# Kernel optimization log

Hardware: AMD Instinct MI355X
Metric: run time of the kernel (lower is better)

## Reference

```python
import jax, jax.numpy as jnp
import numpy as np

SCALE_VALUE = 1  # init kwarg; divide scores by sqrt(scale_value)


def setup_inputs() -> dict:
    key = jax.random.key(0)
    k1, k2 = jax.random.split(key)
    B, S, D = 8, 4096, 128
    inputs = jax.random.normal(k1, (B, S, D), dtype=jnp.float32)
    kernel = jax.random.normal(k2, (3, D, D), dtype=jnp.float32) * 0.05
    return {"inputs": inputs, "kernel": kernel}


def reference(inputs, kernel):
    # Q/K/V projections: [B,S,D] @ [D,D]
    wq = jnp.einsum('bsd,de->bse', inputs, kernel[0])
    wk = jnp.einsum('bsd,de->bse', inputs, kernel[1])
    wv = jnp.einsum('bsd,de->bse', inputs, kernel[2])
    # full attention score matrix [B,S,S], scaled by 1/sqrt(scale_value)
    qk = jnp.einsum('bqd,bkd->bqk', wq, wk) / (SCALE_VALUE ** 0.5)
    attn = jax.nn.softmax(qk, axis=-1)
    v = jnp.einsum('bqk,bkd->bqd', attn, wv)
    # mean pool over sequence -> [B,D]
    return jnp.mean(v, axis=1)
```

## Files before the change

kernel.cpp:

```cpp
#include <hip/hip_runtime.h>

#define Bsz 8
#define Ssz 4096
#define Dsz 128

typedef short bf16x8 __attribute__((ext_vector_type(8)));
typedef float f32x4 __attribute__((ext_vector_type(4)));
typedef float f32x16 __attribute__((ext_vector_type(16)));
typedef int i32x2 __attribute__((ext_vector_type(2)));
typedef int i32x4 __attribute__((ext_vector_type(4)));
typedef unsigned int u32;

union B8 { u32 u[4]; bf16x8 v; };

__device__ __forceinline__ u32 pkbf(float a, float b) {
  u32 ra = __float_as_uint(a) + 0x8000u;
  u32 rb = __float_as_uint(b) + 0x8000u;
  return __builtin_amdgcn_perm(rb, ra, 0x07060302u);
}
__device__ __forceinline__ short f2bf(float f) {
  u32 r = __float_as_uint(f) + 0x8000u;
  return (short)(r >> 16);
}

__device__ __forceinline__ void gll16(const void* g, void* l) {
  __builtin_amdgcn_global_load_lds((const __attribute__((address_space(1))) void*)g,
                                   (__attribute__((address_space(3))) void*)l, 16, 0, 0);
}


__global__ __launch_bounds__(256, 2) void proj_kernel(
    const float* __restrict__ x, const float* __restrict__ wsrc,
    short* __restrict__ Qs, short* __restrict__ Ks, short* __restrict__ Vp) {
  __shared__ short ob[8192];

  const int rb = blockIdx.x;
  const int t = threadIdx.x;
  const int wv = t >> 6, lane = t & 63, l31 = lane & 31, h = lane >> 5;

  bf16x8 xf[2][8];
  {
    const float* xs = x + (size_t)rb * 64 * Dsz;
    #pragma unroll
    for (int st = 0; st < 2; ++st)
      #pragma unroll
      for (int c = 0; c < 8; ++c) {
        const float* p = xs + (st * 32 + l31) * Dsz + c * 16 + 8 * h;
        f32x4 v0 = *(const f32x4*)p;
        f32x4 v1 = *(const f32x4*)(p + 4);
        B8 tmp;
        tmp.u[0] = pkbf(v0[0], v0[1]); tmp.u[1] = pkbf(v0[2], v0[3]);
        tmp.u[2] = pkbf(v1[0], v1[1]); tmp.u[3] = pkbf(v1[2], v1[3]);
        xf[st][c] = tmp.v;
      }
  }

  for (int mat = 0; mat < 3; ++mat) {
    const float* wm = wsrc + (size_t)mat * Dsz * Dsz;
    const float scale = (mat == 0) ? 1.44269504088896340736f : 1.0f;
    bf16x8 wf[8];
    #pragma unroll
    for (int c = 0; c < 8; ++c) {
      const float* p = wm + (size_t)(c * 16 + 8 * h) * Dsz + wv * 32 + l31;
      B8 tmp;
      #pragma unroll
      for (int j = 0; j < 4; ++j)
        tmp.u[j] = pkbf(p[(2 * j) * Dsz] * scale, p[(2 * j + 1) * Dsz] * scale);
      wf[c] = tmp.v;
    }

    if (mat < 2) {
      #pragma unroll
      for (int st = 0; st < 2; ++st) {
        f32x16 acc = {};
        #pragma unroll
        for (int c = 0; c < 8; ++c)
          acc = __builtin_amdgcn_mfma_f32_32x32x16_bf16(wf[c], xf[st][c], acc, 0, 0, 0);
        #pragma unroll
        for (int g = 0; g < 4; ++g) {
          int e0 = wv * 32 + 8 * g + 4 * h;
          int s = st * 32 + l31;
          i32x2 pr;
          pr[0] = pkbf(acc[4 * g + 0], acc[4 * g + 1]);
          pr[1] = pkbf(acc[4 * g + 2], acc[4 * g + 3]);
          *(i32x2*)&ob[(e0 >> 3) * 512 + s * 8 + (e0 & 7)] = pr;
        }
      }
    } else {
      #pragma unroll
      for (int st = 0; st < 2; ++st) {
        f32x16 acc = {};
        #pragma unroll
        for (int c = 0; c < 8; ++c)
          acc = __builtin_amdgcn_mfma_f32_32x32x16_bf16(xf[st][c], wf[c], acc, 0, 0, 0);
        int e = wv * 32 + l31;
        #pragma unroll
        for (int r = 0; r < 16; ++r) {
          int s = st * 32 + (r & 3) + 8 * (r >> 2) + 4 * h;
          ob[s * 128 + e] = f2bf(acc[r]);
        }
      }
    }
    __syncthreads();
    short* dst = (mat == 0 ? Qs : mat == 1 ? Ks : Vp) + (size_t)rb * 8192;
    #pragma unroll
    for (int p = 0; p < 4; ++p)
      *(i32x4*)&dst[(p * 256 + t) * 8] = *(const i32x4*)&ob[(p * 256 + t) * 8];
    __syncthreads();
  }
}

__global__ __launch_bounds__(256, 2) void lsum_kernel(
    const short* __restrict__ Qs, const short* __restrict__ Ks,
    float* __restrict__ lpart) {
  __shared__ short kbuf[2][8192];

  const int b = blockIdx.x, qt = blockIdx.y, kt = blockIdx.z;
  const int t = threadIdx.x;
  const int wv = t >> 6, lane = t & 63, l31 = lane & 31, h = lane >> 5;

  bf16x8 qf[2][8];
  {
    const short* qsrc = Qs + (size_t)(b * 64 + qt * 4 + wv) * 8192;
    #pragma unroll
    for (int nq = 0; nq < 2; ++nq)
      #pragma unroll
      for (int c = 0; c < 8; ++c)
        qf[nq][c] = *(const bf16x8*)&qsrc[(2 * c + h) * 512 + (nq * 32 + l31) * 8];
  }
  float rs2[2] = {0.f, 0.f};

  const char* kbase = (const char*)(Ks + (size_t)(b * 64 + kt * 16) * 8192);
  #define STAGE_K(it_, bf_)                                                     \
    { const char* src_ = kbase + (size_t)(it_) * 16384;                         \
      _Pragma("unroll")                                                         \
      for (int i_ = 0; i_ < 4; ++i_) {                                          \
        int p_ = wv * 4 + i_;                                                   \
        gll16(src_ + p_ * 1024 + lane * 16, (char*)kbuf[bf_] + p_ * 1024);      \
      } }

  STAGE_K(0, 0);
  __syncthreads();

  for (int it = 0; it < 16; ++it) {
    const int cur = it & 1;
    if (it < 15) STAGE_K(it + 1, cur ^ 1);
    #pragma unroll
    for (int mk = 0; mk < 2; ++mk) {
      bf16x8 kf[8];
      #pragma unroll
      for (int c = 0; c < 8; ++c)
        kf[c] = *(const bf16x8*)&kbuf[cur][(2 * c + h) * 512 + (mk * 32 + l31) * 8];
      f32x16 s0 = {}, s1 = {};
      #pragma unroll
      for (int c = 0; c < 8; ++c) {
        s0 = __builtin_amdgcn_mfma_f32_32x32x16_bf16(kf[c], qf[0][c], s0, 0, 0, 0);
        s1 = __builtin_amdgcn_mfma_f32_32x32x16_bf16(kf[c], qf[1][c], s1, 0, 0, 0);
      }
      #pragma unroll
      for (int r = 0; r < 16; ++r) rs2[0] += __builtin_amdgcn_exp2f(s0[r]);
      #pragma unroll
      for (int r = 0; r < 16; ++r) rs2[1] += __builtin_amdgcn_exp2f(s1[r]);
    }
    __syncthreads();
  }

  #pragma unroll
  for (int nq = 0; nq < 2; ++nq) {
    float v = rs2[nq] + __shfl_xor(rs2[nq], 32, 64);
    if (h == 0)
      lpart[((size_t)kt * 8 + b) * 4096 + qt * 256 + wv * 64 + nq * 32 + l31] = v;
  }
}

__global__ __launch_bounds__(256, 2) void attnv_kernel(
    const short* __restrict__ Qs, const short* __restrict__ Ks,
    const short* __restrict__ Vp, const float* __restrict__ lpart,
    float* __restrict__ partials) {
  __shared__ short kbuf[2][8192];
  __shared__ float linv_lds[256];
  __shared__ float gw[4][1024];
  __shared__ float pwb[512];

  const int b = blockIdx.x, qt = blockIdx.y, kt = blockIdx.z;
  const int t = threadIdx.x;
  const int wv = t >> 6, lane = t & 63, l31 = lane & 31, h = lane >> 5;

  {
    int q = qt * 256 + t;
    float l = lpart[(size_t)b * 4096 + q] + lpart[((size_t)1 * 8 + b) * 4096 + q] +
              lpart[((size_t)2 * 8 + b) * 4096 + q] + lpart[((size_t)3 * 8 + b) * 4096 + q];
    linv_lds[t] = 1.f / (l * (float)Ssz);
  }

  bf16x8 qf[2][8];
  {
    const short* qsrc = Qs + (size_t)(b * 64 + qt * 4 + wv) * 8192;
    #pragma unroll
    for (int mq = 0; mq < 2; ++mq)
      #pragma unroll
      for (int c = 0; c < 8; ++c)
        qf[mq][c] = *(const bf16x8*)&qsrc[(2 * c + h) * 512 + (mq * 32 + l31) * 8];
  }
  __syncthreads();

  float li[2][16];
  #pragma unroll
  for (int mq = 0; mq < 2; ++mq)
    #pragma unroll
    for (int r = 0; r < 16; ++r)
      li[mq][r] = linv_lds[wv * 64 + mq * 32 + (r & 3) + 8 * (r >> 2) + 4 * h];

  const char* kbase = (const char*)(Ks + (size_t)(b * 64 + kt * 16) * 8192);
  STAGE_K(0, 0);
  __syncthreads();

  for (int it = 0; it < 16; ++it) {
    const int cur = it & 1;
    if (it < 15) STAGE_K(it + 1, cur ^ 1);
    #pragma unroll
    for (int nk = 0; nk < 2; ++nk) {
      bf16x8 kf[8];
      #pragma unroll
      for (int c = 0; c < 8; ++c)
        kf[c] = *(const bf16x8*)&kbuf[cur][(2 * c + h) * 512 + (nk * 32 + l31) * 8];
      f32x16 s0 = {}, s1 = {};
      #pragma unroll
      for (int c = 0; c < 8; ++c) {
        s0 = __builtin_amdgcn_mfma_f32_32x32x16_bf16(qf[0][c], kf[c], s0, 0, 0, 0);
        s1 = __builtin_amdgcn_mfma_f32_32x32x16_bf16(qf[1][c], kf[c], s1, 0, 0, 0);
      }
      float gp = 0.f;
      #pragma unroll
      for (int r = 0; r < 16; ++r)
        gp += li[0][r] * __builtin_amdgcn_exp2f(s0[r]) +
              li[1][r] * __builtin_amdgcn_exp2f(s1[r]);
      gp += __shfl_xor(gp, 32, 64);
      if (h == 0) gw[wv][it * 64 + nk * 32 + l31] = gp;
    }
    __syncthreads();
  }

  #pragma unroll
  for (int j = 0; j < 4; ++j) {
    int idx = j * 256 + t;
    gw[0][idx] = gw[0][idx] + gw[1][idx] + gw[2][idx] + gw[3][idx];
  }
  __syncthreads();

  {
    const int dp = t & 63, kq = t >> 6;
    const short* vr = Vp + ((size_t)b * 4096 + kt * 1024 + kq * 256) * 128 + 2 * dp;
    float a0 = 0.f, a1 = 0.f;
    #pragma unroll 8
    for (int k = 0; k < 256; ++k) {
      u32 pair = *(const u32*)&vr[(size_t)k * 128];
      float g = gw[0][kq * 256 + k];
      a0 += g * __uint_as_float(pair << 16);
      a1 += g * __uint_as_float(pair & 0xffff0000u);
    }
    pwb[kq * 128 + 2 * dp] = a0;
    pwb[kq * 128 + 2 * dp + 1] = a1;
  }
  __syncthreads();
  if (t < 128) {
    float s = pwb[t] + pwb[128 + t] + pwb[256 + t] + pwb[384 + t];
    partials[((size_t)(qt * 4 + kt) * 8 + b) * 128 + t] = s;
  }
}

__global__ void finalize_kernel(const float* __restrict__ partials, float* __restrict__ out) {
  int i = blockIdx.x * 256 + threadIdx.x;
  if (i < Bsz * Dsz) {
    int b = i >> 7, d = i & 127;
    float s = 0.f;
    #pragma unroll 8
    for (int j = 0; j < 64; ++j) s += partials[((size_t)j * 8 + b) * 128 + d];
    out[i] = s;
  }
}

extern "C" void kernel_launch(void* const* d_in, const int* in_sizes, int n_in,
                              void* d_out, int out_size, void* d_ws, size_t ws_size,
                              hipStream_t stream) {
  const float* x = (const float*)d_in[0];
  const float* w = (const float*)d_in[1];
  short* Qs = (short*)d_ws;
  short* Ks = Qs + (size_t)Bsz * Ssz * Dsz;
  short* Vp = Ks + (size_t)Bsz * Ssz * Dsz;
  float* lpart = (float*)(Vp + (size_t)Bsz * Ssz * Dsz);
  float* partials = lpart + 4 * Bsz * Ssz;

  proj_kernel<<<dim3(Bsz * Ssz / 64), dim3(256), 0, stream>>>(x, w, Qs, Ks, Vp);
  lsum_kernel<<<dim3(Bsz, 16, 4), dim3(256), 0, stream>>>(Qs, Ks, lpart);
  attnv_kernel<<<dim3(Bsz, 16, 4), dim3(256), 0, stream>>>(Qs, Ks, Vp, lpart, partials);
  finalize_kernel<<<dim3(4), dim3(256), 0, stream>>>(partials, (float*)d_out);
}
```

Baseline: 156.6 us.

## Split key range finer and move V weighting into separate atomic GEMV kernel

Doubles the key-dimension split of the row-sum and attention-weight kernels (grid z 4→8, 8 key tiles per block), raising occupancy bounds to increase parallelism. The per-key weight vectors are written to a workspace, and the V-weighted reduction moves from the tail of each attention block into a new GEMV kernel. That kernel sums over query tiles first and then reads V once per batch, accumulating into the output with atomics after a memset. This removes redundant V reads that were repeated across 16 query tiles. In exchange it adds more workspace traffic, an extra launch and nondeterministic atomic summation order.

```diff
diff --git a/kernel.cpp b/kernel.cpp
--- a/kernel.cpp
+++ b/kernel.cpp
@@ -28,6 +28,14 @@
                                    (__attribute__((address_space(3))) void*)l, 16, 0, 0);
 }
 
+
+#define STAGE_K(it_, bf_)                                                     \
+  { const char* src_ = kbase + (size_t)(it_) * 16384;                         \
+    _Pragma("unroll")                                                         \
+    for (int i_ = 0; i_ < 4; ++i_) {                                          \
+      int p_ = wv * 4 + i_;                                                   \
+      gll16(src_ + p_ * 1024 + lane * 16, (char*)kbuf[bf_] + p_ * 1024);      \
+    } }
 
 __global__ __launch_bounds__(256, 2) void proj_kernel(
     const float* __restrict__ x, const float* __restrict__ wsrc,
@@ -110,7 +118,7 @@
   }
 }
 
-__global__ __launch_bounds__(256, 2) void lsum_kernel(
+__global__ __launch_bounds__(256, 4) void lsum_kernel(
     const short* __restrict__ Qs, const short* __restrict__ Ks,
     float* __restrict__ lpart) {
   __shared__ short kbuf[2][8192];
@@ -130,21 +138,13 @@
   }
   float rs2[2] = {0.f, 0.f};
 
-  const char* kbase = (const char*)(Ks + (size_t)(b * 64 + kt * 16) * 8192);
-  #define STAGE_K(it_, bf_)                                                     \
-    { const char* src_ = kbase + (size_t)(it_) * 16384;                         \
-      _Pragma("unroll")                                                         \
-      for (int i_ = 0; i_ < 4; ++i_) {                                          \
-        int p_ = wv * 4 + i_;                                                   \
-        gll16(src_ + p_ * 1024 + lane * 16, (char*)kbuf[bf_] + p_ * 1024);      \
-      } }
-
+  const char* kbase = (const char*)(Ks + (size_t)(b * 64 + kt * 8) * 8192);
   STAGE_K(0, 0);
   __syncthreads();
 
-  for (int it = 0; it < 16; ++it) {
+  for (int it = 0; it < 8; ++it) {
     const int cur = it & 1;
-    if (it < 15) STAGE_K(it + 1, cur ^ 1);
+    if (it < 7) STAGE_K(it + 1, cur ^ 1);
     #pragma unroll
     for (int mk = 0; mk < 2; ++mk) {
       bf16x8 kf[8];
@@ -173,14 +173,12 @@
   }
 }
 
-__global__ __launch_bounds__(256, 2) void attnv_kernel(
+__global__ __launch_bounds__(256, 3) void attnv_kernel(
     const short* __restrict__ Qs, const short* __restrict__ Ks,
-    const short* __restrict__ Vp, const float* __restrict__ lpart,
-    float* __restrict__ partials) {
+    const float* __restrict__ lpart, float* __restrict__ gpart) {
   __shared__ short kbuf[2][8192];
   __shared__ float linv_lds[256];
-  __shared__ float gw[4][1024];
-  __shared__ float pwb[512];
+  __shared__ float gw[4][512];
 
   const int b = blockIdx.x, qt = blockIdx.y, kt = blockIdx.z;
   const int t = threadIdx.x;
@@ -188,8 +186,9 @@
 
   {
     int q = qt * 256 + t;
-    float l = lpart[(size_t)b * 4096 + q] + lpart[((size_t)1 * 8 + b) * 4096 + q] +
-              lpart[((size_t)2 * 8 + b) * 4096 + q] + lpart[((size_t)3 * 8 + b) * 4096 + q];
+    float l = 0.f;
+    #pragma unroll
+    for (int k2 = 0; k2 < 8; ++k2) l += lpart[((size_t)k2 * 8 + b) * 4096 + q];
     linv_lds[t] = 1.f / (l * (float)Ssz);
   }
 
@@ -211,13 +210,13 @@
     for (int r = 0; r < 16; ++r)
       li[mq][r] = linv_lds[wv * 64 + mq * 32 + (r & 3) + 8 * (r >> 2) + 4 * h];
 
-  const char* kbase = (const char*)(Ks + (size_t)(b * 64 + kt * 16) * 8192);
+  const char* kbase = (const char*)(Ks + (size_t)(b * 64 + kt * 8) * 8192);
   STAGE_K(0, 0);
   __syncthreads();
 
-  for (int it = 0; it < 16; ++it) {
+  for (int it = 0; it < 8; ++it) {
     const int cur = it & 1;
-    if (it < 15) STAGE_K(it + 1, cur ^ 1);
+    if (it < 7) STAGE_K(it + 1, cur ^ 1);
     #pragma unroll
     for (int nk = 0; nk < 2; ++nk) {
       bf16x8 kf[8];
@@ -241,42 +240,47 @@
     __syncthreads();
   }
 
+  float* gdst = gpart + (((size_t)(b * 16 + qt) * 8) + kt) * 512;
   #pragma unroll
-  for (int j = 0; j < 4; ++j) {
+  for (int j = 0; j < 2; ++j) {
     int idx = j * 256 + t;
-    gw[0][idx] = gw[0][idx] + gw[1][idx] + gw[2][idx] + gw[3][idx];
-  }
-  __syncthreads();
-
-  {
-    const int dp = t & 63, kq = t >> 6;
-    const short* vr = Vp + ((size_t)b * 4096 + kt * 1024 + kq * 256) * 128 + 2 * dp;
-    float a0 = 0.f, a1 = 0.f;
-    #pragma unroll 8
-    for (int k = 0; k < 256; ++k) {
-      u32 pair = *(const u32*)&vr[(size_t)k * 128];
-      float g = gw[0][kq * 256 + k];
-      a0 += g * __uint_as_float(pair << 16);
-      a1 += g * __uint_as_float(pair & 0xffff0000u);
-    }
-    pwb[kq * 128 + 2 * dp] = a0;
-    pwb[kq * 128 + 2 * dp + 1] = a1;
-  }
-  __syncthreads();
+    gdst[idx] = gw[0][idx] + gw[1][idx] + gw[2][idx] + gw[3][idx];
+  }
+}
+
+__global__ __launch_bounds__(256) void gemv_kernel(
+    const float* __restrict__ gpart, const short* __restrict__ Vp,
+    float* __restrict__ out) {
+  __shared__ float Gs[128];
+  __shared__ float pwb[512];
+  const int b = blockIdx.x, ks = blockIdx.y;
+  const int t = threadIdx.x;
   if (t < 128) {
-    float s = pwb[t] + pwb[128 + t] + pwb[256 + t] + pwb[384 + t];
-    partials[((size_t)(qt * 4 + kt) * 8 + b) * 128 + t] = s;
-  }
-}
-
-__global__ void finalize_kernel(const float* __restrict__ partials, float* __restrict__ out) {
-  int i = blockIdx.x * 256 + threadIdx.x;
-  if (i < Bsz * Dsz) {
-    int b = i >> 7, d = i & 127;
+    int k = ks * 128 + t;
+    int kt = k >> 9, kl = k & 511;
     float s = 0.f;
-    #pragma unroll 8
-    for (int j = 0; j < 64; ++j) s += partials[((size_t)j * 8 + b) * 128 + d];
-    out[i] = s;
+    #pragma unroll
+    for (int qt = 0; qt < 16; ++qt)
+      s += gpart[((size_t)((b * 16 + qt) * 8 + kt)) * 512 + kl];
+    Gs[t] = s;
+  }
+  __syncthreads();
+  const int dp = t & 63, kq = t >> 6;
+  const short* vr = Vp + ((size_t)b * 4096 + ks * 128 + kq * 32) * 128 + 2 * dp;
+  float a0 = 0.f, a1 = 0.f;
+  #pragma unroll 8
+  for (int k = 0; k < 32; ++k) {
+    u32 pair = *(const u32*)&vr[(size_t)k * 128];
+    float g = Gs[kq * 32 + k];
+    a0 += g * __uint_as_float(pair << 16);
+    a1 += g * __uint_as_float(pair & 0xffff0000u);
+  }
+  pwb[kq * 128 + 2 * dp] = a0;
+  pwb[kq * 128 + 2 * dp + 1] = a1;
+  __syncthreads();
+  if (t < 128) {
+    float s = (pwb[t] + pwb[128 + t]) + (pwb[256 + t] + pwb[384 + t]);
+    atomicAdd(&out[b * 128 + t], s);
   }
 }
 
@@ -289,10 +293,11 @@
   short* Ks = Qs + (size_t)Bsz * Ssz * Dsz;
   short* Vp = Ks + (size_t)Bsz * Ssz * Dsz;
   float* lpart = (float*)(Vp + (size_t)Bsz * Ssz * Dsz);
-  float* partials = lpart + 4 * Bsz * Ssz;
-
+  float* gpart = lpart + 8 * Bsz * Ssz;
+
+  hipMemsetAsync(d_out, 0, Bsz * Dsz * sizeof(float), stream);
   proj_kernel<<<dim3(Bsz * Ssz / 64), dim3(256), 0, stream>>>(x, w, Qs, Ks, Vp);
-  lsum_kernel<<<dim3(Bsz, 16, 4), dim3(256), 0, stream>>>(Qs, Ks, lpart);
-  attnv_kernel<<<dim3(Bsz, 16, 4), dim3(256), 0, stream>>>(Qs, Ks, Vp, lpart, partials);
-  finalize_kernel<<<dim3(4), dim3(256), 0, stream>>>(partials, (float*)d_out);
-}
+  lsum_kernel<<<dim3(Bsz, 16, 8), dim3(256), 0, stream>>>(Qs, Ks, lpart);
+  attnv_kernel<<<dim3(Bsz, 16, 8), dim3(256), 0, stream>>>(Qs, Ks, lpart, gpart);
+  gemv_kernel<<<dim3(Bsz, 32), dim3(256), 0, stream>>>(gpart, Vp, (float*)d_out);
+}
```

New measurement: 183.9 us. +17.5%, slower.
